# Kernel optimization log

Measured on AMD Instinct MI355X. Metric: run time of the kernel, lower is better.

Reference implementation:

```python
import jax, jax.numpy as jnp
import numpy as np

D_FFN = 1536
SEQ = 512
N_SLICE = 0
D24 = D_FFN // 24  # 64
EPS = 1e-5

def gelu(x):
    return jax.nn.gelu(x, approximate=False)

def setup_inputs() -> dict:
    key = jax.random.key(0)
    ks = jax.random.split(key, 10)
    B = 32
    x = jax.random.normal(ks[0], (B, SEQ, D_FFN), dtype=jnp.float32)
    # LayerNorm params
    ln_g = jnp.ones((D_FFN,), jnp.float32)
    ln_b = jnp.zeros((D_FFN,), jnp.float32)
    # spatial_cls: Linear(D24->10), Conv1d(SEQ->1,k=1), Linear(10->1)
    w1 = jax.random.normal(ks[1], (D24, 10), jnp.float32) * 0.1
    b1 = jnp.zeros((10,), jnp.float32)
    wc = jax.random.normal(ks[2], (SEQ,), jnp.float32) * 0.04
    bc = jnp.zeros((), jnp.float32)
    w2 = jax.random.normal(ks[3], (10, 1), jnp.float32) * 0.3
    b2 = jnp.zeros((1,), jnp.float32)
    # expert conv1d (kernel size 1) weights: [S_out, S_in]
    Wi = jax.random.normal(ks[4], (SEQ, SEQ), jnp.float32) * 0.04
    bi = -jnp.ones((SEQ,), jnp.float32)   # nn.init.constant_(bias, -1.0)
    Wii = jax.random.normal(ks[5], (SEQ, SEQ), jnp.float32) * 0.04
    bii = jnp.ones((SEQ,), jnp.float32)   # nn.init.constant_(bias, 1.0)
    return {"x": x, "ln_g": ln_g, "ln_b": ln_b, "w1": w1, "b1": b1,
            "wc": wc, "bc": bc, "w2": w2, "b2": b2,
            "Wi": Wi, "bi": bi, "Wii": Wii, "bii": bii}

def reference(x, ln_g, ln_b, w1, b1, wc, bc, w2, b2, Wi, bi, Wii, bii):
    residual = x
    # LayerNorm over d_ffn
    mu = jnp.mean(x, axis=-1, keepdims=True)
    var = jnp.mean((x - mu) ** 2, axis=-1, keepdims=True)
    xn = (x - mu) * jax.lax.rsqrt(var + EPS) * ln_g + ln_b  # [B,S,D]
    # CLS gate: slice -> Linear -> GELU -> Conv1d(S->1,k1) -> GELU -> Linear -> Sigmoid
    c = xn[:, :, N_SLICE * D24:(N_SLICE + 1) * D24]          # [B,S,64]
    h = gelu(jnp.einsum('bsd,dk->bsk', c, w1) + b1)          # [B,S,10]
    h = gelu(jnp.einsum('bsk,s->bk', h, wc) + bc)            # [B,10]
    g = jax.nn.sigmoid(h @ w2 + b2)                          # [B,1]
    idx = jnp.round(jnp.squeeze(g, -1))                      # [B], 0. or 1.
    # hard-routed per-sample conv1d experts (k=1 => [S,S] matmul over seq dim)
    out_i = jnp.einsum('st,btd->bsd', Wi, xn) + bi[:, None]
    out_ii = jnp.einsum('st,btd->bsd', Wii, xn) + bii[:, None]
    out = jnp.where(idx[:, None, None] == 0, out_i, out_ii)
    return gelu(out + residual)
```

## Files before the change

### kernel.cpp

```cpp
#include <hip/hip_runtime.h>
#include <hip/hip_bf16.h>
#include <cstddef>

#define B 32
#define S 512
#define D 1536
#define D24 64
#define EPS 1e-5f

typedef float float4v __attribute__((ext_vector_type(4)));
typedef short short8 __attribute__((ext_vector_type(8)));

__device__ __forceinline__ float gelu_exact(float v) {
    return 0.5f * v * (1.0f + erff(v * 0.70710678118654752440f));
}

__device__ __forceinline__ float gelu_fast(float v) {
    float u = v * v;
    float z = v * __builtin_fmaf(0.07135481627f, u, 1.5957691216f);
    return v / (1.0f + __expf(-z));
}

__device__ __forceinline__ unsigned short f2bf(float f) {
    union { float f; unsigned u; } x; x.f = f;
    unsigned r = x.u + 0x7fffu + ((x.u >> 16) & 1u);
    return (unsigned short)(r >> 16);
}

__global__ __launch_bounds__(256) void stats_kernel(const float* __restrict__ x,
                                                    float* __restrict__ stats) {
    const int lane = threadIdx.x & 63;
    const int w    = threadIdx.x >> 6;
    const int row  = blockIdx.x * 4 + w;
    const float4* xr = (const float4*)(x + (size_t)row * D);
    float s1 = 0.f, s2 = 0.f;
#pragma unroll
    for (int j = 0; j < 6; j++) {
        float4 v = xr[lane + j * 64];
        s1 += v.x + v.y + v.z + v.w;
        s2 += v.x * v.x + v.y * v.y + v.z * v.z + v.w * v.w;
    }
#pragma unroll
    for (int off = 32; off > 0; off >>= 1) {
        s1 += __shfl_down(s1, off, 64);
        s2 += __shfl_down(s2, off, 64);
    }
    if (lane == 0) {
        float mu  = s1 * (1.0f / D);
        float var = s2 * (1.0f / D) - mu * mu;
        stats[row * 2 + 0] = mu;
        stats[row * 2 + 1] = rsqrtf(var + EPS);
    }
}

__global__ __launch_bounds__(256) void convw_kernel(const float* __restrict__ Wi,
                                                    const float* __restrict__ Wii,
                                                    unsigned short* __restrict__ wbf) {
    int i = (blockIdx.x * 256 + threadIdx.x) * 4;
    const float* src = (i < S * S) ? (Wi + i) : (Wii + i - S * S);
    float4 v = *(const float4*)src;
    unsigned short o[4] = {f2bf(v.x), f2bf(v.y), f2bf(v.z), f2bf(v.w)};
    *(uint2*)(wbf + i) = *(const uint2*)o;
}

__global__ __launch_bounds__(256) void nt_kernel(const float* __restrict__ x,
                                                 const float* __restrict__ stats,
                                                 const float* __restrict__ ln_g,
                                                 const float* __restrict__ ln_b,
                                                 unsigned short* __restrict__ xnT,
                                                 float* __restrict__ cbufT) {
    const int b  = blockIdx.z;
    const int t0 = blockIdx.y * 64;
    const int d0 = blockIdx.x * 64;
    const int tid = threadIdx.x;
    __shared__ float tile[64][65];

    const int dq = (tid & 15) * 4;
    const int rg = tid >> 4;
    float4 g4 = *(const float4*)(ln_g + d0 + dq);
    float4 b4 = *(const float4*)(ln_b + d0 + dq);
#pragma unroll
    for (int p = 0; p < 4; p++) {
        int row  = rg + p * 16;
        int grow = b * S + t0 + row;
        float mu   = stats[grow * 2 + 0];
        float rstd = stats[grow * 2 + 1];
        float4 v = *(const float4*)(x + (size_t)grow * D + d0 + dq);
        tile[row][dq + 0] = (v.x - mu) * rstd * g4.x + b4.x;
        tile[row][dq + 1] = (v.y - mu) * rstd * g4.y + b4.y;
        tile[row][dq + 2] = (v.z - mu) * rstd * g4.z + b4.z;
        tile[row][dq + 3] = (v.w - mu) * rstd * g4.w + b4.w;
    }
    __syncthreads();

    const int t8  = (tid & 7) * 8;
    const int dr0 = tid >> 3;
    const bool write_c = (d0 == 0);
#pragma unroll
    for (int p = 0; p < 2; p++) {
        int drow = dr0 + p * 32;
        float fv[8];
        unsigned short bv[8];
#pragma unroll
        for (int j = 0; j < 8; j++) { fv[j] = tile[t8 + j][drow]; bv[j] = f2bf(fv[j]); }
        *(short8*)(xnT + ((size_t)b * D + d0 + drow) * S + t0 + t8) = *(const short8*)bv;
        if (write_c) {
            float* cp = cbufT + ((size_t)b * D24 + drow) * S + t0 + t8;
            *(float4*)(cp + 0) = (float4){fv[0], fv[1], fv[2], fv[3]};
            *(float4*)(cp + 4) = (float4){fv[4], fv[5], fv[6], fv[7]};
        }
    }
}

__global__ __launch_bounds__(256) void gateA_kernel(const float* __restrict__ cbufT,
                                                    const float* __restrict__ w1,
                                                    const float* __restrict__ b1,
                                                    const float* __restrict__ wc,
                                                    float* __restrict__ partial) {
    const int b  = blockIdx.x >> 1;
    const int sb = blockIdx.x & 1;
    const int tid = threadIdx.x;
    const int s = sb * 256 + tid;
    __shared__ float w1s[D24 * 10];
    __shared__ float wsum[4][10];
    for (int i = tid; i < D24 * 10; i += 256) w1s[i] = w1[i];
    __syncthreads();

    float acc[10];
#pragma unroll
    for (int k = 0; k < 10; k++) acc[k] = b1[k];
    const float* cb = cbufT + (size_t)b * D24 * S + s;
#pragma unroll 8
    for (int i = 0; i < D24; i++) {
        float v = cb[(size_t)i * S];
#pragma unroll
        for (int k = 0; k < 10; k++) acc[k] += v * w1s[i * 10 + k];
    }
    float wcs = wc[s];
#pragma unroll
    for (int k = 0; k < 10; k++) {
        float t = gelu_exact(acc[k]) * wcs;
#pragma unroll
        for (int off = 32; off > 0; off >>= 1) t += __shfl_down(t, off, 64);
        if ((tid & 63) == 0) wsum[tid >> 6][k] = t;
    }
    __syncthreads();
    if (tid < 10)
        partial[blockIdx.x * 10 + tid] =
            wsum[0][tid] + wsum[1][tid] + wsum[2][tid] + wsum[3][tid];
}

__global__ __launch_bounds__(64) void gateB_kernel(const float* __restrict__ partial,
                                                   const float* __restrict__ bc,
                                                   const float* __restrict__ w2,
                                                   const float* __restrict__ b2,
                                                   int* __restrict__ sel) {
    int b = threadIdx.x;
    if (b < B) {
        float logit = b2[0];
        float bc0 = bc[0];
#pragma unroll
        for (int k = 0; k < 10; k++) {
            float ssum = partial[(b * 2) * 10 + k] + partial[(b * 2 + 1) * 10 + k];
            logit += gelu_exact(ssum + bc0) * w2[k];
        }
        sel[b] = (logit >= 0.f) ? 1 : 0;
    }
}

__global__ __launch_bounds__(256, 4) void gemm_kernel(const unsigned short* __restrict__ xnT,
                                                      const unsigned short* __restrict__ wbf,
                                                      const int* __restrict__ sel,
                                                      const float* __restrict__ bi,
                                                      const float* __restrict__ bii,
                                                      const float* __restrict__ x,
                                                      float* __restrict__ out) {
    const int b  = blockIdx.z;
    const int s0 = blockIdx.y * 128;
    const int d0 = blockIdx.x * 128;
    const int tid  = threadIdx.x;
    const int lane = tid & 63;
    const int wid  = tid >> 6;
    const int wm = (wid & 1) * 64;
    const int wn = (wid >> 1) * 64;
    const int q   = lane >> 4;
    const int r16 = lane & 15;

    const int ssel = sel[b];
    const unsigned short* W = wbf + (size_t)ssel * S * S;
    const float* bias = ssel ? bii : bi;
    const unsigned short* Xb = xnT + (size_t)b * D * S;

    __shared__ __align__(16) unsigned short As[128 * 64];
    __shared__ __align__(16) unsigned short Bs[128 * 64];

    float4v acc[4][4];
#pragma unroll
    for (int mi = 0; mi < 4; mi++)
#pragma unroll
        for (int ni = 0; ni < 4; ni++) acc[mi][ni] = (float4v){0.f, 0.f, 0.f, 0.f};

    for (int k0 = 0; k0 < S; k0 += 64) {
#pragma unroll
        for (int i = 0; i < 4; i++) {
            int L = i * 256 + tid;
            int row = L >> 3;
            int sc  = L & 7;
            int c16 = sc ^ (row & 7);
            const unsigned short* gaA = W  + (size_t)(s0 + row) * S + k0 + c16 * 8;
            const unsigned short* gaB = Xb + (size_t)(d0 + row) * S + k0 + c16 * 8;
            unsigned short* laA = As + (size_t)(i * 256 + wid * 64) * 8;
            unsigned short* laB = Bs + (size_t)(i * 256 + wid * 64) * 8;
            __builtin_amdgcn_global_load_lds(
                (const __attribute__((address_space(1))) void*)gaA,
                (__attribute__((address_space(3))) void*)laA, 16, 0, 0);
            __builtin_amdgcn_global_load_lds(
                (const __attribute__((address_space(1))) void*)gaB,
                (__attribute__((address_space(3))) void*)laB, 16, 0, 0);
        }
        __syncthreads();

#pragma unroll
        for (int h = 0; h < 2; h++) {
            short8 af[4], bfr[4];
#pragma unroll
            for (int mi = 0; mi < 4; mi++) {
                int row = wm + mi * 16 + r16;
                af[mi] = *(const short8*)(As + row * 64 + (((h << 2) + q) ^ (r16 & 7)) * 8);
            }
#pragma unroll
            for (int ni = 0; ni < 4; ni++) {
                int row = wn + ni * 16 + r16;
                bfr[ni] = *(const short8*)(Bs + row * 64 + (((h << 2) + q) ^ (r16 & 7)) * 8);
            }
#pragma unroll
            for (int mi = 0; mi < 4; mi++)
#pragma unroll
                for (int ni = 0; ni < 4; ni++)
                    acc[mi][ni] = __builtin_amdgcn_mfma_f32_16x16x32_bf16(
                        af[mi], bfr[ni], acc[mi][ni], 0, 0, 0);
        }
        __syncthreads();
    }

#pragma unroll
    for (int mi = 0; mi < 4; mi++) {
        int srow = s0 + wm + mi * 16 + q * 4;
#pragma unroll
        for (int ni = 0; ni < 4; ni++) {
            int d = d0 + wn + ni * 16 + r16;
#pragma unroll
            for (int r = 0; r < 4; r++) {
                int ss = srow + r;
                size_t gi = ((size_t)b * S + ss) * D + d;
                float v = acc[mi][ni][r] + bias[ss] + x[gi];
                out[gi] = gelu_fast(v);
            }
        }
    }
}

extern "C" void kernel_launch(void* const* d_in, const int* in_sizes, int n_in,
                              void* d_out, int out_size, void* d_ws, size_t ws_size,
                              hipStream_t stream) {
    const float* x    = (const float*)d_in[0];
    const float* ln_g = (const float*)d_in[1];
    const float* ln_b = (const float*)d_in[2];
    const float* w1   = (const float*)d_in[3];
    const float* b1   = (const float*)d_in[4];
    const float* wc   = (const float*)d_in[5];
    const float* bc   = (const float*)d_in[6];
    const float* w2   = (const float*)d_in[7];
    const float* b2   = (const float*)d_in[8];
    const float* Wi   = (const float*)d_in[9];
    const float* bi   = (const float*)d_in[10];
    const float* Wii  = (const float*)d_in[11];
    const float* bii  = (const float*)d_in[12];
    float* out = (float*)d_out;

    char* ws = (char*)d_ws;
    const size_t XNT_BYTES   = (size_t)B * D * S * 2;
    const size_t STATS_BYTES = (size_t)B * S * 2 * 4;
    const size_t C_BYTES     = (size_t)B * D24 * S * 4;
    const size_t WBF_BYTES   = (size_t)2 * S * S * 2;
    const size_t PART_BYTES  = (size_t)B * 2 * 10 * 4;
    unsigned short* xnT   = (unsigned short*)ws;
    float*          stat  = (float*)(ws + XNT_BYTES);
    float*          cbufT = (float*)(ws + XNT_BYTES + STATS_BYTES);
    unsigned short* wbf   = (unsigned short*)(ws + XNT_BYTES + STATS_BYTES + C_BYTES);
    float*          part  = (float*)(ws + XNT_BYTES + STATS_BYTES + C_BYTES + WBF_BYTES);
    int*            sel   = (int*)(ws + XNT_BYTES + STATS_BYTES + C_BYTES + WBF_BYTES + PART_BYTES);

    stats_kernel<<<(B * S) / 4, 256, 0, stream>>>(x, stat);
    convw_kernel<<<(2 * S * S) / 1024, 256, 0, stream>>>(Wi, Wii, wbf);
    nt_kernel<<<dim3(D / 64, S / 64, B), 256, 0, stream>>>(x, stat, ln_g, ln_b, xnT, cbufT);
    gateA_kernel<<<B * 2, 256, 0, stream>>>(cbufT, w1, b1, wc, part);
    gateB_kernel<<<1, 64, 0, stream>>>(part, bc, w2, b2, sel);
    gemm_kernel<<<dim3(D / 128, S / 128, B), 256, 0, stream>>>(xnT, wbf, sel, bi, bii, x, out);
}
```

Before: 305.6 us.

## Fuse LayerNorm stats into transpose kernel and double-buffer GEMM LDS tiles

Merges the row-statistics kernel and the normalize/transpose kernel into a single ln_kernel. Each block computes mean and rstd for 64 rows, then walks all 24 d-tiles, so the stats buffer and one launch go away. The GEMM gains a two-stage LDS ping-pong that issues the next K tile's global_load_lds before computing the current one, with launch bounds relaxed to 2 blocks per CU to make room for the doubled shared memory. The risks are that ln_kernel launches only 256 blocks, each running a long serial loop, and that the GEMM loop now relies on the loop-end barrier to order the async loads against buffer reuse.

```diff
diff --git a/kernel.cpp b/kernel.cpp
--- a/kernel.cpp
+++ b/kernel.cpp
@@ -27,29 +27,80 @@
     return (unsigned short)(r >> 16);
 }
 
-__global__ __launch_bounds__(256) void stats_kernel(const float* __restrict__ x,
-                                                    float* __restrict__ stats) {
-    const int lane = threadIdx.x & 63;
-    const int w    = threadIdx.x >> 6;
-    const int row  = blockIdx.x * 4 + w;
-    const float4* xr = (const float4*)(x + (size_t)row * D);
-    float s1 = 0.f, s2 = 0.f;
-#pragma unroll
-    for (int j = 0; j < 6; j++) {
-        float4 v = xr[lane + j * 64];
-        s1 += v.x + v.y + v.z + v.w;
-        s2 += v.x * v.x + v.y * v.y + v.z * v.z + v.w * v.w;
-    }
-#pragma unroll
-    for (int off = 32; off > 0; off >>= 1) {
-        s1 += __shfl_down(s1, off, 64);
-        s2 += __shfl_down(s2, off, 64);
-    }
-    if (lane == 0) {
-        float mu  = s1 * (1.0f / D);
-        float var = s2 * (1.0f / D) - mu * mu;
-        stats[row * 2 + 0] = mu;
-        stats[row * 2 + 1] = rsqrtf(var + EPS);
+__global__ __launch_bounds__(256) void ln_kernel(const float* __restrict__ x,
+                                                 const float* __restrict__ ln_g,
+                                                 const float* __restrict__ ln_b,
+                                                 unsigned short* __restrict__ xnT,
+                                                 float* __restrict__ cbufT) {
+    const int b  = blockIdx.y;
+    const int t0 = blockIdx.x * 64;
+    const int tid  = threadIdx.x;
+    const int lane = tid & 63;
+    const int w    = tid >> 6;
+
+    __shared__ float tile[64][65];
+    __shared__ float lmu[64], lrs[64];
+
+    for (int r = 0; r < 16; r++) {
+        int row = w * 16 + r;
+        const float4* xr = (const float4*)(x + ((size_t)(b * S + t0 + row)) * D);
+        float s1 = 0.f, s2 = 0.f;
+#pragma unroll
+        for (int j = 0; j < 6; j++) {
+            float4 v = xr[lane + j * 64];
+            s1 += v.x + v.y + v.z + v.w;
+            s2 += v.x * v.x + v.y * v.y + v.z * v.z + v.w * v.w;
+        }
+#pragma unroll
+        for (int off = 32; off > 0; off >>= 1) {
+            s1 += __shfl_down(s1, off, 64);
+            s2 += __shfl_down(s2, off, 64);
+        }
+        if (lane == 0) {
+            float mu  = s1 * (1.0f / D);
+            float var = s2 * (1.0f / D) - mu * mu;
+            lmu[row] = mu;
+            lrs[row] = rsqrtf(var + EPS);
+        }
+    }
+    __syncthreads();
+
+    const int dq = (tid & 15) * 4;
+    const int rg = tid >> 4;
+    const int t8  = (tid & 7) * 8;
+    const int dr0 = tid >> 3;
+
+    for (int dt = 0; dt < 24; dt++) {
+        const int d0 = dt * 64;
+        float4 g4 = *(const float4*)(ln_g + d0 + dq);
+        float4 b4 = *(const float4*)(ln_b + d0 + dq);
+#pragma unroll
+        for (int p = 0; p < 4; p++) {
+            int row  = rg + p * 16;
+            float mu   = lmu[row];
+            float rstd = lrs[row];
+            float4 v = *(const float4*)(x + ((size_t)(b * S + t0 + row)) * D + d0 + dq);
+            tile[row][dq + 0] = (v.x - mu) * rstd * g4.x + b4.x;
+            tile[row][dq + 1] = (v.y - mu) * rstd * g4.y + b4.y;
+            tile[row][dq + 2] = (v.z - mu) * rstd * g4.z + b4.z;
+            tile[row][dq + 3] = (v.w - mu) * rstd * g4.w + b4.w;
+        }
+        __syncthreads();
+#pragma unroll
+        for (int p = 0; p < 2; p++) {
+            int drow = dr0 + p * 32;
+            float fv[8];
+            unsigned short bv[8];
+#pragma unroll
+            for (int j = 0; j < 8; j++) { fv[j] = tile[t8 + j][drow]; bv[j] = f2bf(fv[j]); }
+            *(short8*)(xnT + ((size_t)b * D + d0 + drow) * S + t0 + t8) = *(const short8*)bv;
+            if (dt == 0) {
+                float* cp = cbufT + ((size_t)b * D24 + drow) * S + t0 + t8;
+                *(float4*)(cp + 0) = (float4){fv[0], fv[1], fv[2], fv[3]};
+                *(float4*)(cp + 4) = (float4){fv[4], fv[5], fv[6], fv[7]};
+            }
+        }
+        __syncthreads();
     }
 }
 
@@ -61,55 +112,6 @@
     float4 v = *(const float4*)src;
     unsigned short o[4] = {f2bf(v.x), f2bf(v.y), f2bf(v.z), f2bf(v.w)};
     *(uint2*)(wbf + i) = *(const uint2*)o;
-}
-
-__global__ __launch_bounds__(256) void nt_kernel(const float* __restrict__ x,
-                                                 const float* __restrict__ stats,
-                                                 const float* __restrict__ ln_g,
-                                                 const float* __restrict__ ln_b,
-                                                 unsigned short* __restrict__ xnT,
-                                                 float* __restrict__ cbufT) {
-    const int b  = blockIdx.z;
-    const int t0 = blockIdx.y * 64;
-    const int d0 = blockIdx.x * 64;
-    const int tid = threadIdx.x;
-    __shared__ float tile[64][65];
-
-    const int dq = (tid & 15) * 4;
-    const int rg = tid >> 4;
-    float4 g4 = *(const float4*)(ln_g + d0 + dq);
-    float4 b4 = *(const float4*)(ln_b + d0 + dq);
-#pragma unroll
-    for (int p = 0; p < 4; p++) {
-        int row  = rg + p * 16;
-        int grow = b * S + t0 + row;
-        float mu   = stats[grow * 2 + 0];
-        float rstd = stats[grow * 2 + 1];
-        float4 v = *(const float4*)(x + (size_t)grow * D + d0 + dq);
-        tile[row][dq + 0] = (v.x - mu) * rstd * g4.x + b4.x;
-        tile[row][dq + 1] = (v.y - mu) * rstd * g4.y + b4.y;
-        tile[row][dq + 2] = (v.z - mu) * rstd * g4.z + b4.z;
-        tile[row][dq + 3] = (v.w - mu) * rstd * g4.w + b4.w;
-    }
-    __syncthreads();
-
-    const int t8  = (tid & 7) * 8;
-    const int dr0 = tid >> 3;
-    const bool write_c = (d0 == 0);
-#pragma unroll
-    for (int p = 0; p < 2; p++) {
-        int drow = dr0 + p * 32;
-        float fv[8];
-        unsigned short bv[8];
-#pragma unroll
-        for (int j = 0; j < 8; j++) { fv[j] = tile[t8 + j][drow]; bv[j] = f2bf(fv[j]); }
-        *(short8*)(xnT + ((size_t)b * D + d0 + drow) * S + t0 + t8) = *(const short8*)bv;
-        if (write_c) {
-            float* cp = cbufT + ((size_t)b * D24 + drow) * S + t0 + t8;
-            *(float4*)(cp + 0) = (float4){fv[0], fv[1], fv[2], fv[3]};
-            *(float4*)(cp + 4) = (float4){fv[4], fv[5], fv[6], fv[7]};
-        }
-    }
 }
 
 __global__ __launch_bounds__(256) void gateA_kernel(const float* __restrict__ cbufT,
@@ -168,7 +170,7 @@
     }
 }
 
-__global__ __launch_bounds__(256, 4) void gemm_kernel(const unsigned short* __restrict__ xnT,
+__global__ __launch_bounds__(256, 2) void gemm_kernel(const unsigned short* __restrict__ xnT,
                                                       const unsigned short* __restrict__ wbf,
                                                       const int* __restrict__ sel,
                                                       const float* __restrict__ bi,
@@ -191,16 +193,10 @@
     const float* bias = ssel ? bii : bi;
     const unsigned short* Xb = xnT + (size_t)b * D * S;
 
-    __shared__ __align__(16) unsigned short As[128 * 64];
-    __shared__ __align__(16) unsigned short Bs[128 * 64];
-
-    float4v acc[4][4];
-#pragma unroll
-    for (int mi = 0; mi < 4; mi++)
-#pragma unroll
-        for (int ni = 0; ni < 4; ni++) acc[mi][ni] = (float4v){0.f, 0.f, 0.f, 0.f};
-
-    for (int k0 = 0; k0 < S; k0 += 64) {
+    __shared__ __align__(16) unsigned short As[2][128 * 64];
+    __shared__ __align__(16) unsigned short Bs[2][128 * 64];
+
+    auto stage = [&](int k0, int bf) {
 #pragma unroll
         for (int i = 0; i < 4; i++) {
             int L = i * 256 + tid;
@@ -209,8 +205,8 @@
             int c16 = sc ^ (row & 7);
             const unsigned short* gaA = W  + (size_t)(s0 + row) * S + k0 + c16 * 8;
             const unsigned short* gaB = Xb + (size_t)(d0 + row) * S + k0 + c16 * 8;
-            unsigned short* laA = As + (size_t)(i * 256 + wid * 64) * 8;
-            unsigned short* laB = Bs + (size_t)(i * 256 + wid * 64) * 8;
+            unsigned short* laA = As[bf] + (size_t)(i * 256 + wid * 64) * 8;
+            unsigned short* laB = Bs[bf] + (size_t)(i * 256 + wid * 64) * 8;
             __builtin_amdgcn_global_load_lds(
                 (const __attribute__((address_space(1))) void*)gaA,
                 (__attribute__((address_space(3))) void*)laA, 16, 0, 0);
@@ -218,20 +214,35 @@
                 (const __attribute__((address_space(1))) void*)gaB,
                 (__attribute__((address_space(3))) void*)laB, 16, 0, 0);
         }
-        __syncthreads();
-
+    };
+
+    float4v acc[4][4];
+#pragma unroll
+    for (int mi = 0; mi < 4; mi++)
+#pragma unroll
+        for (int ni = 0; ni < 4; ni++) acc[mi][ni] = (float4v){0.f, 0.f, 0.f, 0.f};
+
+    stage(0, 0);
+    __syncthreads();
+
+    for (int it = 0; it < 8; it++) {
+        const int cur = it & 1;
+        if (it < 7) stage((it + 1) * 64, cur ^ 1);
+
+        const unsigned short* Ac = As[cur];
+        const unsigned short* Bc = Bs[cur];
 #pragma unroll
         for (int h = 0; h < 2; h++) {
             short8 af[4], bfr[4];
 #pragma unroll
             for (int mi = 0; mi < 4; mi++) {
                 int row = wm + mi * 16 + r16;
-                af[mi] = *(const short8*)(As + row * 64 + (((h << 2) + q) ^ (r16 & 7)) * 8);
+                af[mi] = *(const short8*)(Ac + row * 64 + (((h << 2) + q) ^ (r16 & 7)) * 8);
             }
 #pragma unroll
             for (int ni = 0; ni < 4; ni++) {
                 int row = wn + ni * 16 + r16;
-                bfr[ni] = *(const short8*)(Bs + row * 64 + (((h << 2) + q) ^ (r16 & 7)) * 8);
+                bfr[ni] = *(const short8*)(Bc + row * 64 + (((h << 2) + q) ^ (r16 & 7)) * 8);
             }
 #pragma unroll
             for (int mi = 0; mi < 4; mi++)
@@ -280,20 +291,17 @@
 
     char* ws = (char*)d_ws;
     const size_t XNT_BYTES   = (size_t)B * D * S * 2;
-    const size_t STATS_BYTES = (size_t)B * S * 2 * 4;
     const size_t C_BYTES     = (size_t)B * D24 * S * 4;
     const size_t WBF_BYTES   = (size_t)2 * S * S * 2;
     const size_t PART_BYTES  = (size_t)B * 2 * 10 * 4;
     unsigned short* xnT   = (unsigned short*)ws;
-    float*          stat  = (float*)(ws + XNT_BYTES);
-    float*          cbufT = (float*)(ws + XNT_BYTES + STATS_BYTES);
-    unsigned short* wbf   = (unsigned short*)(ws + XNT_BYTES + STATS_BYTES + C_BYTES);
-    float*          part  = (float*)(ws + XNT_BYTES + STATS_BYTES + C_BYTES + WBF_BYTES);
-    int*            sel   = (int*)(ws + XNT_BYTES + STATS_BYTES + C_BYTES + WBF_BYTES + PART_BYTES);
-
-    stats_kernel<<<(B * S) / 4, 256, 0, stream>>>(x, stat);
+    float*          cbufT = (float*)(ws + XNT_BYTES);
+    unsigned short* wbf   = (unsigned short*)(ws + XNT_BYTES + C_BYTES);
+    float*          part  = (float*)(ws + XNT_BYTES + C_BYTES + WBF_BYTES);
+    int*            sel   = (int*)(ws + XNT_BYTES + C_BYTES + WBF_BYTES + PART_BYTES);
+
+    ln_kernel<<<dim3(S / 64, B), 256, 0, stream>>>(x, ln_g, ln_b, xnT, cbufT);
     convw_kernel<<<(2 * S * S) / 1024, 256, 0, stream>>>(Wi, Wii, wbf);
-    nt_kernel<<<dim3(D / 64, S / 64, B), 256, 0, stream>>>(x, stat, ln_g, ln_b, xnT, cbufT);
     gateA_kernel<<<B * 2, 256, 0, stream>>>(cbufT, w1, b1, wc, part);
     gateB_kernel<<<1, 64, 0, stream>>>(part, bc, w2, b2, sel);
     gemm_kernel<<<dim3(D / 128, S / 128, B), 256, 0, stream>>>(xnT, wbf, sel, bi, bii, x, out);
```

Measured after the change: 288.0 us. -5.8%, faster.

## Double-buffer GEMM LDS tiles with BK=32 and swap grid axes

Applied to the files above, without the earlier changes.

The GEMM main loop now uses two LDS buffers with a K-step of 32 instead of one buffer with a K-step of 64. The next tile's global-to-LDS load is issued before the MFMAs on the current tile, so load latency can overlap compute, and there is one barrier per step instead of two. The LDS swizzle pattern is changed to match the 4-chunk rows. The grid now puts the S tiles on x so blocks sharing the same xnT d-tile run together, the min-occupancy launch bound is dropped, and convw is launched after nt. The cost is more loop iterations and barriers overall, plus possible register or occupancy changes.

```diff
diff --git a/kernel.cpp b/kernel.cpp
--- a/kernel.cpp
+++ b/kernel.cpp
@@ -51,16 +51,6 @@
         stats[row * 2 + 0] = mu;
         stats[row * 2 + 1] = rsqrtf(var + EPS);
     }
-}
-
-__global__ __launch_bounds__(256) void convw_kernel(const float* __restrict__ Wi,
-                                                    const float* __restrict__ Wii,
-                                                    unsigned short* __restrict__ wbf) {
-    int i = (blockIdx.x * 256 + threadIdx.x) * 4;
-    const float* src = (i < S * S) ? (Wi + i) : (Wii + i - S * S);
-    float4 v = *(const float4*)src;
-    unsigned short o[4] = {f2bf(v.x), f2bf(v.y), f2bf(v.z), f2bf(v.w)};
-    *(uint2*)(wbf + i) = *(const uint2*)o;
 }
 
 __global__ __launch_bounds__(256) void nt_kernel(const float* __restrict__ x,
@@ -110,6 +100,16 @@
             *(float4*)(cp + 4) = (float4){fv[4], fv[5], fv[6], fv[7]};
         }
     }
+}
+
+__global__ __launch_bounds__(256) void convw_kernel(const float* __restrict__ Wi,
+                                                    const float* __restrict__ Wii,
+                                                    unsigned short* __restrict__ wbf) {
+    int i = (blockIdx.x * 256 + threadIdx.x) * 4;
+    const float* src = (i < S * S) ? (Wi + i) : (Wii + i - S * S);
+    float4 v = *(const float4*)src;
+    unsigned short o[4] = {f2bf(v.x), f2bf(v.y), f2bf(v.z), f2bf(v.w)};
+    *(uint2*)(wbf + i) = *(const uint2*)o;
 }
 
 __global__ __launch_bounds__(256) void gateA_kernel(const float* __restrict__ cbufT,
@@ -168,16 +168,16 @@
     }
 }
 
-__global__ __launch_bounds__(256, 4) void gemm_kernel(const unsigned short* __restrict__ xnT,
-                                                      const unsigned short* __restrict__ wbf,
-                                                      const int* __restrict__ sel,
-                                                      const float* __restrict__ bi,
-                                                      const float* __restrict__ bii,
-                                                      const float* __restrict__ x,
-                                                      float* __restrict__ out) {
+__global__ __launch_bounds__(256) void gemm_kernel(const unsigned short* __restrict__ xnT,
+                                                   const unsigned short* __restrict__ wbf,
+                                                   const int* __restrict__ sel,
+                                                   const float* __restrict__ bi,
+                                                   const float* __restrict__ bii,
+                                                   const float* __restrict__ x,
+                                                   float* __restrict__ out) {
     const int b  = blockIdx.z;
-    const int s0 = blockIdx.y * 128;
-    const int d0 = blockIdx.x * 128;
+    const int s0 = blockIdx.x * 128;
+    const int d0 = blockIdx.y * 128;
     const int tid  = threadIdx.x;
     const int lane = tid & 63;
     const int wid  = tid >> 6;
@@ -191,26 +191,20 @@
     const float* bias = ssel ? bii : bi;
     const unsigned short* Xb = xnT + (size_t)b * D * S;
 
-    __shared__ __align__(16) unsigned short As[128 * 64];
-    __shared__ __align__(16) unsigned short Bs[128 * 64];
-
-    float4v acc[4][4];
-#pragma unroll
-    for (int mi = 0; mi < 4; mi++)
-#pragma unroll
-        for (int ni = 0; ni < 4; ni++) acc[mi][ni] = (float4v){0.f, 0.f, 0.f, 0.f};
-
-    for (int k0 = 0; k0 < S; k0 += 64) {
-#pragma unroll
-        for (int i = 0; i < 4; i++) {
+    __shared__ __align__(16) unsigned short As[2][128 * 32];
+    __shared__ __align__(16) unsigned short Bs[2][128 * 32];
+
+    auto stage = [&](int k0, int bf) {
+#pragma unroll
+        for (int i = 0; i < 2; i++) {
             int L = i * 256 + tid;
-            int row = L >> 3;
-            int sc  = L & 7;
-            int c16 = sc ^ (row & 7);
+            int row = L >> 2;
+            int sc  = L & 3;
+            int c16 = sc ^ ((row >> 1) & 3);
             const unsigned short* gaA = W  + (size_t)(s0 + row) * S + k0 + c16 * 8;
             const unsigned short* gaB = Xb + (size_t)(d0 + row) * S + k0 + c16 * 8;
-            unsigned short* laA = As + (size_t)(i * 256 + wid * 64) * 8;
-            unsigned short* laB = Bs + (size_t)(i * 256 + wid * 64) * 8;
+            unsigned short* laA = As[bf] + (size_t)(i * 256 + wid * 64) * 8;
+            unsigned short* laB = Bs[bf] + (size_t)(i * 256 + wid * 64) * 8;
             __builtin_amdgcn_global_load_lds(
                 (const __attribute__((address_space(1))) void*)gaA,
                 (__attribute__((address_space(3))) void*)laA, 16, 0, 0);
@@ -218,28 +212,42 @@
                 (const __attribute__((address_space(1))) void*)gaB,
                 (__attribute__((address_space(3))) void*)laB, 16, 0, 0);
         }
-        __syncthreads();
-
-#pragma unroll
-        for (int h = 0; h < 2; h++) {
-            short8 af[4], bfr[4];
-#pragma unroll
-            for (int mi = 0; mi < 4; mi++) {
-                int row = wm + mi * 16 + r16;
-                af[mi] = *(const short8*)(As + row * 64 + (((h << 2) + q) ^ (r16 & 7)) * 8);
-            }
-#pragma unroll
-            for (int ni = 0; ni < 4; ni++) {
-                int row = wn + ni * 16 + r16;
-                bfr[ni] = *(const short8*)(Bs + row * 64 + (((h << 2) + q) ^ (r16 & 7)) * 8);
-            }
-#pragma unroll
-            for (int mi = 0; mi < 4; mi++)
-#pragma unroll
-                for (int ni = 0; ni < 4; ni++)
-                    acc[mi][ni] = __builtin_amdgcn_mfma_f32_16x16x32_bf16(
-                        af[mi], bfr[ni], acc[mi][ni], 0, 0, 0);
-        }
+    };
+
+    float4v acc[4][4];
+#pragma unroll
+    for (int mi = 0; mi < 4; mi++)
+#pragma unroll
+        for (int ni = 0; ni < 4; ni++) acc[mi][ni] = (float4v){0.f, 0.f, 0.f, 0.f};
+
+    stage(0, 0);
+    __syncthreads();
+
+    for (int it = 0; it < 16; it++) {
+        const int cur = it & 1;
+        if (it < 15) stage((it + 1) * 32, cur ^ 1);
+
+        const unsigned short* Ac = As[cur];
+        const unsigned short* Bc = Bs[cur];
+        short8 af[4], bfr[4];
+#pragma unroll
+        for (int mi = 0; mi < 4; mi++) {
+            int row = wm + mi * 16 + r16;
+            int slot = q ^ ((row >> 1) & 3);
+            af[mi] = *(const short8*)(Ac + (row * 4 + slot) * 8);
+        }
+#pragma unroll
+        for (int ni = 0; ni < 4; ni++) {
+            int row = wn + ni * 16 + r16;
+            int slot = q ^ ((row >> 1) & 3);
+            bfr[ni] = *(const short8*)(Bc + (row * 4 + slot) * 8);
+        }
+#pragma unroll
+        for (int mi = 0; mi < 4; mi++)
+#pragma unroll
+            for (int ni = 0; ni < 4; ni++)
+                acc[mi][ni] = __builtin_amdgcn_mfma_f32_16x16x32_bf16(
+                    af[mi], bfr[ni], acc[mi][ni], 0, 0, 0);
         __syncthreads();
     }
 
@@ -292,9 +300,9 @@
     int*            sel   = (int*)(ws + XNT_BYTES + STATS_BYTES + C_BYTES + WBF_BYTES + PART_BYTES);
 
     stats_kernel<<<(B * S) / 4, 256, 0, stream>>>(x, stat);
+    nt_kernel<<<dim3(D / 64, S / 64, B), 256, 0, stream>>>(x, stat, ln_g, ln_b, xnT, cbufT);
     convw_kernel<<<(2 * S * S) / 1024, 256, 0, stream>>>(Wi, Wii, wbf);
-    nt_kernel<<<dim3(D / 64, S / 64, B), 256, 0, stream>>>(x, stat, ln_g, ln_b, xnT, cbufT);
     gateA_kernel<<<B * 2, 256, 0, stream>>>(cbufT, w1, b1, wc, part);
     gateB_kernel<<<1, 64, 0, stream>>>(part, bc, w2, b2, sel);
-    gemm_kernel<<<dim3(D / 128, S / 128, B), 256, 0, stream>>>(xnT, wbf, sel, bi, bii, x, out);
-}
+    gemm_kernel<<<dim3(S / 128, D / 128, B), 256, 0, stream>>>(xnT, wbf, sel, bi, bii, x, out);
+}
```

Result: no change. 310.3 us (+1.5%).
